# Optimization experiments

Measured on AMD Instinct MI355X. Metric: run time of the kernel, lower is better.

The kernel has to match this reference:

```python
import jax, jax.numpy as jnp
import numpy as np
from jax.scipy.special import gammaln

LENF = 15  # gamma unit-hydrograph length (UH_gamma default-ish routing window)
DT = 1.0


def setup_inputs() -> dict:
    key = jax.random.key(0)
    k = jax.random.split(key, 6)
    nb, nt, npar, nmul = 2000, 365, 12, 8
    return {
        "P": jax.random.uniform(k[0], (nb, nt), jnp.float32) * 10.0,   # precip mm/day
        "Ep": jax.random.uniform(k[1], (nb, nt), jnp.float32) * 5.0,   # PET mm/day
        "Tair": jax.random.normal(k[2], (nb, nt), jnp.float32) * 8.0,  # air temp C
        "params": jax.random.uniform(k[3], (nb, nt, npar, nmul), jnp.float32),  # raw [0,1]
        "rout_a": jax.random.uniform(k[4], (nb,), jnp.float32),
        "rout_b": jax.random.uniform(k[5], (nb,), jnp.float32),
    }


def reference(P, Ep, Tair, params, rout_a, rout_b):
    # P, Ep, Tair: [nb, nt]; params: [nb, nt, 12, nmul] raw in [0,1]
    nb, nt = P.shape
    nmul = params.shape[-1]
    dtype = P.dtype

    xs = (P.T, Ep.T, Tair.T, jnp.transpose(params, (1, 0, 2, 3)))  # time-major
    S0 = jnp.full((nb, nmul), 0.5, dtype)
    carry0 = (S0, S0, S0, S0, S0)  # snow, interception, soil, interflow, baseflow stores

    def step(carry, inp):
        S1, S2, S3, S4, S5 = carry
        Pt, Ept, Tt, pr = inp
        Pt, Ept, Tt = Pt[:, None], Ept[:, None], Tt[:, None]  # broadcast over nmul
        # parameter scaling (param_bounds: raw*(hi-lo)+lo), all [nb, nmul]
        tt    = -3.0 + pr[:, 0] * 8.0      # temp threshold
        ddf   = pr[:, 1] * 20.0            # degree-day melt factor
        Smax3 = 20.0 + pr[:, 3] * 680.0    # soil capacity
        p_lo  = 0.005 + pr[:, 4] * 0.99    # saturation_8 low frac
        p_hi  = 0.005 + pr[:, 5] * 0.99    # saturation_8 high frac
        p_exp = 1.0 + pr[:, 6] * 4.0       # recharge_2 exponent
        i1    = pr[:, 8]                   # interflow_4 linear coef
        i2    = pr[:, 9] * 1e-3            # interflow_4 quadratic coef
        kb    = pr[:, 10]                  # baseflow_1 coef

        # snowfall_1 / rainfall_1 via smoothThreshold_temperature_logistic (hard indicator)
        snowfrac = (Tt <= tt).astype(dtype)
        snow = Pt * snowfrac
        rain = Pt * (1.0 - snowfrac)
        # melt_1
        melt = jnp.clip(jnp.minimum(ddf * (Tt - tt), S1 / DT), 0.0)
        S1n = S1 + snow - melt
        # interception_1: In*(1 - smoothThreshold_storage_logistic)=In*0.95
        inter = rain * (1.0 - 0.05)
        # evap_1
        evap2 = jnp.minimum(S2 / DT, Ept)
        S2n = jnp.clip(S2 + (rain - inter) - evap2, 0.0)
        infil = melt + inter
        # saturation_8
        satexc = (p_lo + (p_hi - p_lo) * jnp.clip(S3, 0.0) / Smax3) * infil
        # effective_1
        rem = jnp.clip(infil - satexc, 0.0)
        # recharge_2
        rech = rem * (jnp.clip(S3, 0.0) / Smax3) ** p_exp
        # evap_7
        evap3 = jnp.minimum(jnp.clip(S3, 0.0) / Smax3 * Ept, S3 / DT)
        S3n = S3 + rem - rech - evap3
        # interflow_4
        S4c = jnp.clip(S4, 0.0)
        iflow = jnp.minimum(S4c, i1 * S4c + i2 * S4c ** 2)
        S4n = S4 + rech - iflow
        # baseflow_1
        base = kb * S5
        S5n = S5 + iflow - base
        Q = (satexc + base).mean(-1)  # average over nmul ensemble -> [nb]
        return (S1n, S2n, S3n, S4n, S5n), Q

    _, Q = jax.lax.scan(step, carry0, xs)  # Q: [nt, nb]
    Q = Q.T  # [nb, nt]

    # UH_gamma routing weights, normalized over lenF
    aa = jax.nn.relu(rout_a * 2.9) + 0.1   # [nb]
    th = jax.nn.relu(rout_b * 6.5) + 0.5
    t = jnp.arange(LENF, dtype=dtype)[:, None] + 0.5  # [lenF, 1], matches arange(0.5, lenF)
    denom = jnp.exp(gammaln(aa)) * th ** aa
    w = (1.0 / denom) * t ** (aa - 1.0) * jnp.exp(-t / th)  # [lenF, nb]
    w = w / w.sum(0)

    # UH_conv: grouped causal conv1d (flipped kernel, pad m-1, trim right)
    def causal_conv(q, wb):
        return jnp.convolve(q, wb, mode="full")[: q.shape[0]]

    Qrout = jax.vmap(causal_conv)(Q, w.T)  # [nb, nt]
    return Qrout
```

## Files before the change

kernel.cpp:

```cpp
#include <hip/hip_runtime.h>

#define NB      2000
#define NT      365
#define LENF    15
#define PSTRIDE 96
#define CH      16
#define NFULL   22
#define NCHUNK  23
#define CHBYTES (CH * PSTRIDE * 4)
#define BASIN_BYTES (NT * PSTRIDE * 4)
#define CLAMP16     (BASIN_BYTES - 16)
#define PARW    1544
#define FRCW    72

#define GLD16(g, l) __builtin_amdgcn_global_load_lds( \
    (const __attribute__((address_space(1))) void*)(g), \
    (__attribute__((address_space(3))) void*)(l), 16, 0, 0)
#define GLD4(g, l) __builtin_amdgcn_global_load_lds( \
    (const __attribute__((address_space(1))) void*)(g), \
    (__attribute__((address_space(3))) void*)(l), 4, 0, 0)

#define EXP2F(x) __builtin_amdgcn_exp2f(x)
#define LOG2F(x) __builtin_amdgcn_logf(x)
#define LOG2E    1.44269504088896f

template <int CTRL>
__device__ __forceinline__ float dpp_mov(float x) {
  int xi = __float_as_int(x);
  int r  = __builtin_amdgcn_update_dpp(xi, xi, CTRL, 0xF, 0xF, true);
  return __int_as_float(r);
}
#define DPP_XOR1   0xB1
#define DPP_XOR2   0x4E
#define DPP_HMIRR  0x141

__global__ __launch_bounds__(64) void prms_kernel(
    const float* __restrict__ P, const float* __restrict__ Ep,
    const float* __restrict__ Tair, const float* __restrict__ params,
    const float* __restrict__ rout_a, const float* __restrict__ rout_b,
    float* __restrict__ out)
{
  __shared__ __attribute__((aligned(16))) float sh_par[2][2 * PARW];
  __shared__ __attribute__((aligned(16))) float sh_frc[2][2][FRCW];
  __shared__ float Qs[2][NT + 3];

  const int lane = threadIdx.x;
  const int m    = lane & 7;
  const int bsel = (lane >> 3) & 1;
  const int b0   = blockIdx.x * 2;

  const float ra0 = rout_a[b0],     rb0 = rout_b[b0];
  const float ra1 = rout_a[b0 + 1], rb1 = rout_b[b0 + 1];

  const char* pbg[2] = {
    (const char*)(params + (size_t)b0 * (NT * PSTRIDE)),
    (const char*)(params + (size_t)(b0 + 1) * (NT * PSTRIDE)) };

  const int farr = (lane >> 4) > 2 ? 2 : (lane >> 4);
  const int fs   = lane & 15;
  const float* fsrcs[2][3] = {
    { P + (size_t)b0 * NT,       Ep + (size_t)b0 * NT,       Tair + (size_t)b0 * NT },
    { P + (size_t)(b0 + 1) * NT, Ep + (size_t)(b0 + 1) * NT, Tair + (size_t)(b0 + 1) * NT } };

  auto ISSUE = [&](int c, int buf) {
    #pragma unroll
    for (int bs = 0; bs < 2; ++bs) {
      #pragma unroll
      for (int j = 0; j < 6; ++j) {
        int off = c * CHBYTES + j * 1024 + lane * 16;
        off = off > CLAMP16 ? CLAMP16 : off;
        GLD16(pbg[bs] + off, &sh_par[buf][bs * PARW + j * 256]);
      }
    }
    #pragma unroll
    for (int bs = 0; bs < 2; ++bs) {
      int ft = c * CH + fs;
      ft = ft > NT - 1 ? NT - 1 : ft;
      GLD4(fsrcs[bs][farr] + ft, &sh_frc[buf][bs][0]);
    }
  };

  float S1 = 0.5f, S2 = 0.5f, S3 = 0.5f, S4 = 0.5f, S5 = 0.5f;
  const int pbase = bsel * PARW + m;
  const int fbb   = bsel * FRCW;

  auto LOADB = [&](int buf, int s0, float r[4][12]) {
    #pragma unroll
    for (int k = 0; k < 4; ++k) {
      const float* par = &sh_par[buf][pbase + (s0 + k) * PSTRIDE];
      r[k][0] = par[0];   r[k][1] = par[8];   r[k][2] = par[24];
      r[k][3] = par[32];  r[k][4] = par[40];  r[k][5] = par[48];
      r[k][6] = par[64];  r[k][7] = par[72];  r[k][8] = par[80];
      const float* f = &sh_frc[buf][0][fbb];
      r[k][9]  = f[s0 + k];
      r[k][10] = f[16 + s0 + k];
      r[k][11] = f[32 + s0 + k];
    }
  };

  auto STEPD = [&](const float* d, int t) {
    const float tt    = fmaf(d[0], 8.0f, -3.0f);
    const float ddf   = d[1] * 20.0f;
    const float Smax3 = fmaf(d[2], 680.0f, 20.0f);
    const float p_lo  = fmaf(d[3], 0.99f, 0.005f);
    const float p_hi  = fmaf(d[4], 0.99f, 0.005f);
    const float p_exp = fmaf(d[5], 4.0f, 1.0f);
    const float i1    = d[6];
    const float i2    = d[7] * 0.001f;
    const float kb    = d[8];
    const float Pt    = d[9];
    const float Ept   = d[10];
    const float Tt    = d[11];

    const float snow = (Tt <= tt) ? Pt : 0.0f;
    const float rain = Pt - snow;
    const float melt = fmaxf(fminf(ddf * (Tt - tt), S1), 0.0f);
    S1 = S1 + snow - melt;

    const float inter = rain * 0.95f;
    const float evap2 = fminf(S2, Ept);
    S2 = fmaxf(S2 + (rain - inter) - evap2, 0.0f);

    const float infil  = melt + inter;
    const float frac   = fmaxf(S3, 0.0f) * __builtin_amdgcn_rcpf(Smax3);
    const float satexc = (p_lo + (p_hi - p_lo) * frac) * infil;
    const float rem    = fmaxf(infil - satexc, 0.0f);
    const float rech   = rem * EXP2F(p_exp * LOG2F(frac));
    const float evap3  = fminf(frac * Ept, S3);
    S3 = S3 + rem - rech - evap3;

    const float S4c   = fmaxf(S4, 0.0f);
    const float iflow = fminf(S4c, fmaf(i2, S4c * S4c, i1 * S4c));
    S4 = S4 + rech - iflow;

    const float base = kb * S5;
    S5 = S5 + iflow - base;

    float q = satexc + base;
    q += dpp_mov<DPP_XOR1>(q);
    q += dpp_mov<DPP_XOR2>(q);
    q += dpp_mov<DPP_HMIRR>(q);
    if ((lane & 55) == 0)
      Qs[bsel][t] = q * 0.125f;
  };

  float rA[4][12], rB[4][12];
  auto STEP4 = [&](float r[4][12], int tb) {
    #pragma unroll
    for (int k = 0; k < 4; ++k) STEPD(r[k], tb + k);
  };

  ISSUE(0, 0);
  ISSUE(1, 1);
  for (int c = 0; c < NFULL; ++c) {
    asm volatile("s_waitcnt vmcnt(14)" ::: "memory");
    const int buf = c & 1;
    const int t0  = c * CH;
    LOADB(buf, 0,  rA);
    LOADB(buf, 4,  rB);  STEP4(rA, t0);
    LOADB(buf, 8,  rA);  STEP4(rB, t0 + 4);
    LOADB(buf, 12, rB);  STEP4(rA, t0 + 8);
    STEP4(rB, t0 + 12);
    asm volatile("s_waitcnt lgkmcnt(0)" ::: "memory");
    if (c + 2 < NCHUNK) ISSUE(c + 2, buf);
  }
  asm volatile("s_waitcnt vmcnt(0)" ::: "memory");
  {
    const int t0 = NFULL * CH;
    LOADB(0, 0, rA);
    LOADB(0, 4, rB);  STEP4(rA, t0);
    LOADB(0, 8, rA);  STEP4(rB, t0 + 4);
    STEP4(rA, t0 + 8);
    float d12[12];
    {
      const float* par = &sh_par[0][pbase + 12 * PSTRIDE];
      d12[0] = par[0];  d12[1] = par[8];  d12[2] = par[24];
      d12[3] = par[32]; d12[4] = par[40]; d12[5] = par[48];
      d12[6] = par[64]; d12[7] = par[72]; d12[8] = par[80];
      const float* f = &sh_frc[0][0][fbb];
      d12[9] = f[12]; d12[10] = f[28]; d12[11] = f[44];
    }
    STEPD(d12, t0 + 12);
  }

  __syncthreads();

  #pragma unroll
  for (int bs = 0; bs < 2; ++bs) {
    const float ra_v = bs ? ra1 : ra0;
    const float rb_v = bs ? rb1 : rb0;
    const float aa  = fmaxf(ra_v * 2.9f, 0.0f) + 0.1f;
    const float th  = fmaxf(rb_v * 6.5f, 0.0f) + 0.5f;
    const float am1 = aa - 1.0f;
    const float ith = -LOG2E / th;

    float w[LENF];
    float wsum = 0.0f;
    #pragma unroll
    for (int j = 0; j < LENF; ++j) {
      const float tj = (float)j + 0.5f;
      w[j] = EXP2F(fmaf(am1, LOG2F(tj), tj * ith));
      wsum += w[j];
    }
    const float inv = 1.0f / wsum;
    #pragma unroll
    for (int j = 0; j < LENF; ++j) w[j] *= inv;

    float* __restrict__ ob = out + (size_t)(b0 + bs) * NT;
    #pragma unroll
    for (int k = 0; k < 6; ++k) {
      const int t = lane + k * 64;
      if (t < NT) {
        float acc = 0.0f;
        #pragma unroll
        for (int j = 0; j < LENF; ++j) {
          const int idx = t - j;
          if (idx >= 0) acc += w[j] * Qs[bs][idx];
        }
        ob[t] = acc;
      }
    }
  }
}

extern "C" void kernel_launch(void* const* d_in, const int* in_sizes, int n_in,
                              void* d_out, int out_size, void* d_ws, size_t ws_size,
                              hipStream_t stream) {
  const float* P      = (const float*)d_in[0];
  const float* Ep     = (const float*)d_in[1];
  const float* Tair   = (const float*)d_in[2];
  const float* params = (const float*)d_in[3];
  const float* ra     = (const float*)d_in[4];
  const float* rb     = (const float*)d_in[5];
  float* out = (float*)d_out;

  prms_kernel<<<NB / 2, 64, 0, stream>>>(P, Ep, Tair, params, ra, rb, out);
}
```

Baseline: 80.74 us.

## Pack four basins per wavefront and use per-step double-buffered LDS reads

Each 64-lane wavefront now handles four basins instead of two, using 32 of its lanes instead of 16, and the grid is halved to NB/4 blocks. The parameter and forcing prefetch issues twice as many global-to-LDS loads per chunk, and the wait count is raised to match. The per-step LDS reads change from four-step register batches to a two-slot scheme that loads the next step while the current one computes. The aim is to fill more of each wave and cut the number of serial-recurrence waves, at the cost of more LDS per block (fewer blocks per CU), fewer blocks overall, and less latency hiding in the register prefetch.

After: 94.01 us. 16.4% more time.

```diff
diff --git a/kernel.cpp b/kernel.cpp
--- a/kernel.cpp
+++ b/kernel.cpp
@@ -12,6 +12,7 @@
 #define CLAMP16     (BASIN_BYTES - 16)
 #define PARW    1544
 #define FRCW    72
+#define NBW     4
 
 #define GLD16(g, l) __builtin_amdgcn_global_load_lds( \
     (const __attribute__((address_space(1))) void*)(g), \
@@ -40,31 +41,36 @@
     const float* __restrict__ rout_a, const float* __restrict__ rout_b,
     float* __restrict__ out)
 {
-  __shared__ __attribute__((aligned(16))) float sh_par[2][2 * PARW];
-  __shared__ __attribute__((aligned(16))) float sh_frc[2][2][FRCW];
-  __shared__ float Qs[2][NT + 3];
+  __shared__ __attribute__((aligned(16))) float sh_par[2][NBW * PARW];
+  __shared__ __attribute__((aligned(16))) float sh_frc[2][NBW][FRCW];
+  __shared__ float Qs[NBW][NT + 3];
 
   const int lane = threadIdx.x;
   const int m    = lane & 7;
-  const int bsel = (lane >> 3) & 1;
-  const int b0   = blockIdx.x * 2;
-
-  const float ra0 = rout_a[b0],     rb0 = rout_b[b0];
-  const float ra1 = rout_a[b0 + 1], rb1 = rout_b[b0 + 1];
-
-  const char* pbg[2] = {
-    (const char*)(params + (size_t)b0 * (NT * PSTRIDE)),
-    (const char*)(params + (size_t)(b0 + 1) * (NT * PSTRIDE)) };
+  const int bsel = (lane >> 3) & 3;
+  const int b0   = blockIdx.x * NBW;
+
+  float ra[NBW], rb[NBW];
+  #pragma unroll
+  for (int bs = 0; bs < NBW; ++bs) { ra[bs] = rout_a[b0 + bs]; rb[bs] = rout_b[b0 + bs]; }
+
+  const char* pbg[NBW];
+  #pragma unroll
+  for (int bs = 0; bs < NBW; ++bs)
+    pbg[bs] = (const char*)(params + (size_t)(b0 + bs) * (NT * PSTRIDE));
 
   const int farr = (lane >> 4) > 2 ? 2 : (lane >> 4);
   const int fs   = lane & 15;
-  const float* fsrcs[2][3] = {
-    { P + (size_t)b0 * NT,       Ep + (size_t)b0 * NT,       Tair + (size_t)b0 * NT },
-    { P + (size_t)(b0 + 1) * NT, Ep + (size_t)(b0 + 1) * NT, Tair + (size_t)(b0 + 1) * NT } };
+  const float* fptr[NBW];
+  #pragma unroll
+  for (int bs = 0; bs < NBW; ++bs) {
+    const float* base = (farr == 0) ? P : (farr == 1) ? Ep : Tair;
+    fptr[bs] = base + (size_t)(b0 + bs) * NT;
+  }
 
   auto ISSUE = [&](int c, int buf) {
     #pragma unroll
-    for (int bs = 0; bs < 2; ++bs) {
+    for (int bs = 0; bs < NBW; ++bs) {
       #pragma unroll
       for (int j = 0; j < 6; ++j) {
         int off = c * CHBYTES + j * 1024 + lane * 16;
@@ -73,29 +79,25 @@
       }
     }
     #pragma unroll
-    for (int bs = 0; bs < 2; ++bs) {
+    for (int bs = 0; bs < NBW; ++bs) {
       int ft = c * CH + fs;
       ft = ft > NT - 1 ? NT - 1 : ft;
-      GLD4(fsrcs[bs][farr] + ft, &sh_frc[buf][bs][0]);
+      GLD4(fptr[bs] + ft, &sh_frc[buf][bs][0]);
     }
   };
 
   float S1 = 0.5f, S2 = 0.5f, S3 = 0.5f, S4 = 0.5f, S5 = 0.5f;
   const int pbase = bsel * PARW + m;
-  const int fbb   = bsel * FRCW;
-
-  auto LOADB = [&](int buf, int s0, float r[4][12]) {
-    #pragma unroll
-    for (int k = 0; k < 4; ++k) {
-      const float* par = &sh_par[buf][pbase + (s0 + k) * PSTRIDE];
-      r[k][0] = par[0];   r[k][1] = par[8];   r[k][2] = par[24];
-      r[k][3] = par[32];  r[k][4] = par[40];  r[k][5] = par[48];
-      r[k][6] = par[64];  r[k][7] = par[72];  r[k][8] = par[80];
-      const float* f = &sh_frc[buf][0][fbb];
-      r[k][9]  = f[s0 + k];
-      r[k][10] = f[16 + s0 + k];
-      r[k][11] = f[32 + s0 + k];
-    }
+
+  auto LOADR = [&](int buf, int s, float* r) {
+    const float* par = &sh_par[buf][pbase + s * PSTRIDE];
+    r[0] = par[0];   r[1] = par[8];   r[2] = par[24];
+    r[3] = par[32];  r[4] = par[40];  r[5] = par[48];
+    r[6] = par[64];  r[7] = par[72];  r[8] = par[80];
+    const float* f = &sh_frc[buf][bsel][0];
+    r[9]  = f[s];
+    r[10] = f[16 + s];
+    r[11] = f[32 + s];
   };
 
   auto STEPD = [&](const float* d, int t) {
@@ -140,57 +142,43 @@
     q += dpp_mov<DPP_XOR1>(q);
     q += dpp_mov<DPP_XOR2>(q);
     q += dpp_mov<DPP_HMIRR>(q);
-    if ((lane & 55) == 0)
+    if ((lane & 39) == 0)
       Qs[bsel][t] = q * 0.125f;
   };
 
-  float rA[4][12], rB[4][12];
-  auto STEP4 = [&](float r[4][12], int tb) {
-    #pragma unroll
-    for (int k = 0; k < 4; ++k) STEPD(r[k], tb + k);
-  };
-
+  float r[2][12];
   ISSUE(0, 0);
   ISSUE(1, 1);
   for (int c = 0; c < NFULL; ++c) {
-    asm volatile("s_waitcnt vmcnt(14)" ::: "memory");
+    asm volatile("s_waitcnt vmcnt(28)" ::: "memory");
     const int buf = c & 1;
     const int t0  = c * CH;
-    LOADB(buf, 0,  rA);
-    LOADB(buf, 4,  rB);  STEP4(rA, t0);
-    LOADB(buf, 8,  rA);  STEP4(rB, t0 + 4);
-    LOADB(buf, 12, rB);  STEP4(rA, t0 + 8);
-    STEP4(rB, t0 + 12);
+    LOADR(buf, 0, r[0]);
+    #pragma unroll
+    for (int s = 0; s < CH; ++s) {
+      if (s < CH - 1) LOADR(buf, s + 1, r[(s + 1) & 1]);
+      STEPD(r[s & 1], t0 + s);
+    }
     asm volatile("s_waitcnt lgkmcnt(0)" ::: "memory");
     if (c + 2 < NCHUNK) ISSUE(c + 2, buf);
   }
   asm volatile("s_waitcnt vmcnt(0)" ::: "memory");
   {
     const int t0 = NFULL * CH;
-    LOADB(0, 0, rA);
-    LOADB(0, 4, rB);  STEP4(rA, t0);
-    LOADB(0, 8, rA);  STEP4(rB, t0 + 4);
-    STEP4(rA, t0 + 8);
-    float d12[12];
-    {
-      const float* par = &sh_par[0][pbase + 12 * PSTRIDE];
-      d12[0] = par[0];  d12[1] = par[8];  d12[2] = par[24];
-      d12[3] = par[32]; d12[4] = par[40]; d12[5] = par[48];
-      d12[6] = par[64]; d12[7] = par[72]; d12[8] = par[80];
-      const float* f = &sh_frc[0][0][fbb];
-      d12[9] = f[12]; d12[10] = f[28]; d12[11] = f[44];
-    }
-    STEPD(d12, t0 + 12);
+    LOADR(0, 0, r[0]);
+    #pragma unroll
+    for (int s = 0; s < 13; ++s) {
+      if (s < 12) LOADR(0, s + 1, r[(s + 1) & 1]);
+      STEPD(r[s & 1], t0 + s);
+    }
   }
 
   __syncthreads();
 
   #pragma unroll
-  for (int bs = 0; bs < 2; ++bs) {
-    const float ra_v = bs ? ra1 : ra0;
-    const float rb_v = bs ? rb1 : rb0;
-    const float aa  = fmaxf(ra_v * 2.9f, 0.0f) + 0.1f;
-    const float th  = fmaxf(rb_v * 6.5f, 0.0f) + 0.5f;
+  for (int bs = 0; bs < NBW; ++bs) {
+    const float aa  = fmaxf(ra[bs] * 2.9f, 0.0f) + 0.1f;
+    const float th  = fmaxf(rb[bs] * 6.5f, 0.0f) + 0.5f;
     const float am1 = aa - 1.0f;
     const float ith = -LOG2E / th;
 
@@ -234,5 +222,5 @@
   const float* rb     = (const float*)d_in[5];
   float* out = (float*)d_out;
 
-  prms_kernel<<<NB / 2, 64, 0, stream>>>(P, Ep, Tair, params, ra, rb, out);
+  prms_kernel<<<NB / NBW, 64, 0, stream>>>(P, Ep, Tair, params, ra, rb, out);
 }
```

## Replace LDS double-buffered async staging with direct register prefetch from global

Applied to the files above, without the earlier changes.

Drops the global_load_lds double-buffer pipeline, which staged per-chunk parameter and forcing data in shared memory. Each lane now loads its own parameters and forcings straight from global memory into a rotating 4-deep register ring, prefetching four timesteps ahead. This removes the LDS traffic, the manual waitcnt handling and the shared buffers. In exchange the loads are scattered 4-byte global reads, and latency hiding now depends only on a short prefetch distance inside a serial recurrence.

Measured after the change: 92.30 us. +14.3%, slower.

```diff
diff --git a/kernel.cpp b/kernel.cpp
--- a/kernel.cpp
+++ b/kernel.cpp
@@ -4,21 +4,6 @@
 #define NT      365
 #define LENF    15
 #define PSTRIDE 96
-#define CH      16
-#define NFULL   22
-#define NCHUNK  23
-#define CHBYTES (CH * PSTRIDE * 4)
-#define BASIN_BYTES (NT * PSTRIDE * 4)
-#define CLAMP16     (BASIN_BYTES - 16)
-#define PARW    1544
-#define FRCW    72
-
-#define GLD16(g, l) __builtin_amdgcn_global_load_lds( \
-    (const __attribute__((address_space(1))) void*)(g), \
-    (__attribute__((address_space(3))) void*)(l), 16, 0, 0)
-#define GLD4(g, l) __builtin_amdgcn_global_load_lds( \
-    (const __attribute__((address_space(1))) void*)(g), \
-    (__attribute__((address_space(3))) void*)(l), 4, 0, 0)
 
 #define EXP2F(x) __builtin_amdgcn_exp2f(x)
 #define LOG2F(x) __builtin_amdgcn_logf(x)
@@ -40,62 +25,36 @@
     const float* __restrict__ rout_a, const float* __restrict__ rout_b,
     float* __restrict__ out)
 {
-  __shared__ __attribute__((aligned(16))) float sh_par[2][2 * PARW];
-  __shared__ __attribute__((aligned(16))) float sh_frc[2][2][FRCW];
   __shared__ float Qs[2][NT + 3];
 
   const int lane = threadIdx.x;
   const int m    = lane & 7;
   const int bsel = (lane >> 3) & 1;
   const int b0   = blockIdx.x * 2;
+  const int b    = b0 + bsel;
 
   const float ra0 = rout_a[b0],     rb0 = rout_b[b0];
   const float ra1 = rout_a[b0 + 1], rb1 = rout_b[b0 + 1];
 
-  const char* pbg[2] = {
-    (const char*)(params + (size_t)b0 * (NT * PSTRIDE)),
-    (const char*)(params + (size_t)(b0 + 1) * (NT * PSTRIDE)) };
-
-  const int farr = (lane >> 4) > 2 ? 2 : (lane >> 4);
-  const int fs   = lane & 15;
-  const float* fsrcs[2][3] = {
-    { P + (size_t)b0 * NT,       Ep + (size_t)b0 * NT,       Tair + (size_t)b0 * NT },
-    { P + (size_t)(b0 + 1) * NT, Ep + (size_t)(b0 + 1) * NT, Tair + (size_t)(b0 + 1) * NT } };
-
-  auto ISSUE = [&](int c, int buf) {
-    #pragma unroll
-    for (int bs = 0; bs < 2; ++bs) {
-      #pragma unroll
-      for (int j = 0; j < 6; ++j) {
-        int off = c * CHBYTES + j * 1024 + lane * 16;
-        off = off > CLAMP16 ? CLAMP16 : off;
-        GLD16(pbg[bs] + off, &sh_par[buf][bs * PARW + j * 256]);
-      }
-    }
-    #pragma unroll
-    for (int bs = 0; bs < 2; ++bs) {
-      int ft = c * CH + fs;
-      ft = ft > NT - 1 ? NT - 1 : ft;
-      GLD4(fsrcs[bs][farr] + ft, &sh_frc[buf][bs][0]);
-    }
-  };
+  const float* pl = params + (size_t)b * (NT * PSTRIDE) + m;
+  const float* fP = P    + (size_t)b * NT;
+  const float* fE = Ep   + (size_t)b * NT;
+  const float* fT = Tair + (size_t)b * NT;
 
   float S1 = 0.5f, S2 = 0.5f, S3 = 0.5f, S4 = 0.5f, S5 = 0.5f;
-  const int pbase = bsel * PARW + m;
-  const int fbb   = bsel * FRCW;
 
-  auto LOADB = [&](int buf, int s0, float r[4][12]) {
-    #pragma unroll
-    for (int k = 0; k < 4; ++k) {
-      const float* par = &sh_par[buf][pbase + (s0 + k) * PSTRIDE];
-      r[k][0] = par[0];   r[k][1] = par[8];   r[k][2] = par[24];
-      r[k][3] = par[32];  r[k][4] = par[40];  r[k][5] = par[48];
-      r[k][6] = par[64];  r[k][7] = par[72];  r[k][8] = par[80];
-      const float* f = &sh_frc[buf][0][fbb];
-      r[k][9]  = f[s0 + k];
-      r[k][10] = f[16 + s0 + k];
-      r[k][11] = f[32 + s0 + k];
-    }
+  float rr[4][12];
+
+  auto LOADP = [&](float* r, const float* lp, int so) {
+    const float* q = lp + so * PSTRIDE;
+    r[0] = q[0];   r[1] = q[8];   r[2] = q[24];
+    r[3] = q[32];  r[4] = q[40];  r[5] = q[48];
+    r[6] = q[64];  r[7] = q[72];  r[8] = q[80];
+  };
+  auto LOADF = [&](float* r, const float* p0, const float* p1, const float* p2, int o) {
+    r[9]  = p0[o];
+    r[10] = p1[o];
+    r[11] = p2[o];
   };
 
   auto STEPD = [&](const float* d, int t) {
@@ -144,43 +103,36 @@
       Qs[bsel][t] = q * 0.125f;
   };
 
-  float rA[4][12], rB[4][12];
-  auto STEP4 = [&](float r[4][12], int tb) {
+  #pragma unroll
+  for (int s = 0; s < 4; ++s) {
+    LOADP(rr[s], pl, s);
+    LOADF(rr[s], fP, fE, fT, s);
+  }
+
+  const float* gp = pl;
+  for (int g = 0; g < 45; ++g) {
+    const int t0 = g * 8;
+    const float* gp4 = gp + 4 * PSTRIDE;
+    const float* gp8 = gp + 8 * PSTRIDE;
     #pragma unroll
-    for (int k = 0; k < 4; ++k) STEPD(r[k], tb + k);
-  };
-
-  ISSUE(0, 0);
-  ISSUE(1, 1);
-  for (int c = 0; c < NFULL; ++c) {
-    asm volatile("s_waitcnt vmcnt(14)" ::: "memory");
-    const int buf = c & 1;
-    const int t0  = c * CH;
-    LOADB(buf, 0,  rA);
-    LOADB(buf, 4,  rB);  STEP4(rA, t0);
-    LOADB(buf, 8,  rA);  STEP4(rB, t0 + 4);
-    LOADB(buf, 12, rB);  STEP4(rA, t0 + 8);
-    STEP4(rB, t0 + 12);
-    asm volatile("s_waitcnt lgkmcnt(0)" ::: "memory");
-    if (c + 2 < NCHUNK) ISSUE(c + 2, buf);
+    for (int s = 0; s < 8; ++s) {
+      STEPD(rr[s & 3], t0 + s);
+      if (s < 4) LOADP(rr[s & 3], gp4, s);
+      else       LOADP(rr[s & 3], gp8, s - 4);
+      LOADF(rr[s & 3], fP, fE, fT, s + 4);
+    }
+    gp += 8 * PSTRIDE; fP += 8; fE += 8; fT += 8;
   }
-  asm volatile("s_waitcnt vmcnt(0)" ::: "memory");
   {
-    const int t0 = NFULL * CH;
-    LOADB(0, 0, rA);
-    LOADB(0, 4, rB);  STEP4(rA, t0);
-    LOADB(0, 8, rA);  STEP4(rB, t0 + 4);
-    STEP4(rA, t0 + 8);
-    float d12[12];
-    {
-      const float* par = &sh_par[0][pbase + 12 * PSTRIDE];
-      d12[0] = par[0];  d12[1] = par[8];  d12[2] = par[24];
-      d12[3] = par[32]; d12[4] = par[40]; d12[5] = par[48];
-      d12[6] = par[64]; d12[7] = par[72]; d12[8] = par[80];
-      const float* f = &sh_frc[0][0][fbb];
-      d12[9] = f[12]; d12[10] = f[28]; d12[11] = f[44];
+    const float* gp4 = gp + 4 * PSTRIDE;
+    #pragma unroll
+    for (int s = 0; s < 5; ++s) {
+      STEPD(rr[s & 3], 360 + s);
+      if (s == 0) {
+        LOADP(rr[0], gp4, 0);
+        LOADF(rr[0], fP, fE, fT, 4);
+      }
     }
-    STEPD(d12, t0 + 12);
   }
 
   __syncthreads();
```
